# Performance work log

Measured on AMD Instinct MI355X. Metric: run time of the kernel, lower is better.

The kernel has to match this reference:

```python
import jax, jax.numpy as jnp
import numpy as np

MOE_TOPK = 2


def setup_inputs() -> dict:
    key = jax.random.key(0)
    k1, k2 = jax.random.split(key, 2)
    hidden_states = jax.random.normal(k1, (4, 4096, 2048), dtype=jnp.float32)
    gate_w = jax.random.normal(k2, (2048, 64), dtype=jnp.float32) * 0.02
    gate_b = jnp.zeros((64,), dtype=jnp.float32)
    return {"hidden_states": hidden_states, "gate_w": gate_w, "gate_b": gate_b}


def reference(hidden_states, gate_w, gate_b):
    # flatten [B, S, D] -> [N, D]
    x = hidden_states.reshape(-1, hidden_states.shape[-1])
    # gate linear: [N, E]
    logits = jnp.einsum("nd,de->ne", x, gate_w) + gate_b
    # stable softmax; torch detaches the max (no grad through max path)
    logits_max = jax.lax.stop_gradient(jnp.max(logits, axis=-1, keepdims=True))
    probs = jax.nn.softmax(logits - logits_max, axis=-1)
    # top-k selection + renormalize
    topk_vals, topk_idx = jax.lax.top_k(probs, MOE_TOPK)
    if MOE_TOPK == 1:
        norm_vals = jnp.ones_like(topk_vals)
    else:
        sum_vals = jnp.clip(jnp.sum(topk_vals, axis=-1, keepdims=True), 1e-6, None)
        norm_vals = topk_vals / sum_vals
    return logits, norm_vals, topk_idx
```

## Files before the change

kernel.cpp:

```cpp
#include <hip/hip_runtime.h>
#include <hip/hip_bf16.h>

#define NTOK 16384
#define DIM  2048
#define NE   64
#define TPB  32
#define NTILE 2
#define KG   8
#define KPW  (DIM / KG)
#define KSTEPS (KPW / 32)
#define NKS_ALL (DIM / 32)
#define LP   65

typedef __attribute__((ext_vector_type(8))) short  short8;
typedef __attribute__((ext_vector_type(4))) float  f32x4;

static __device__ __forceinline__ unsigned short f2bf(float f) {
    unsigned u = __float_as_uint(f);
    unsigned r = (u + 0x7fffu + ((u >> 16) & 1u)) >> 16;
    return (unsigned short)r;
}
static __device__ __forceinline__ float bf2f(unsigned short h) {
    return __uint_as_float(((unsigned)h) << 16);
}

static __device__ __forceinline__ void cvt_pair(float x0, float x1,
                                                unsigned& hi, unsigned& lo) {
    union { __hip_bfloat162 b; unsigned u; } h, l;
    h.b = __float22bfloat162_rn(float2{x0, x1});
    float h0 = __uint_as_float(h.u << 16);
    float h1 = __uint_as_float(h.u & 0xffff0000u);
    l.b = __float22bfloat162_rn(float2{x0 - h0, x1 - h1});
    hi = h.u; lo = l.u;
}

__global__ void pack_w(const float* __restrict__ W,
                       unsigned short* __restrict__ WH,
                       unsigned short* __restrict__ WL) {
    int idx = blockIdx.x * 256 + threadIdx.x;
    if (idx >= DIM * NE) return;
    int k = idx / NE, e = idx % NE;
    float w = W[idx];
    unsigned short h = f2bf(w);
    unsigned short l = f2bf(w - bf2f(h));
    int etile = e >> 4, col = e & 15;
    int kstep = k >> 5, lsub = (k >> 3) & 3, j = k & 7;
    size_t off = (((size_t)etile * NKS_ALL + kstep) * 64 + (lsub * 16 + col)) * 8 + j;
    WH[off] = h;
    WL[off] = l;
}

__global__ __launch_bounds__(512, 4) void router_mfma(
    const float* __restrict__ X,
    const unsigned short* __restrict__ WH,
    const unsigned short* __restrict__ WL,
    const float* __restrict__ B, float* __restrict__ out)
{
    __shared__ float red[KG][TPB][LP];
    __shared__ float lg[TPB][LP];

    const int tid  = threadIdx.x;
    const int lane = tid & 63;
    const int kg   = __builtin_amdgcn_readfirstlane(tid >> 6);
    const int t0   = blockIdx.x * TPB;

    const int arow = lane & 15;
    const int koff = (lane >> 4) * 8;

    const float* xp0 = X + (size_t)(t0 + arow) * DIM + kg * KPW + koff;
    const float* xp1 = xp0 + (size_t)16 * DIM;

    f32x4 acc[NTILE][4];
#pragma unroll
    for (int t = 0; t < NTILE; ++t)
#pragma unroll
        for (int et = 0; et < 4; ++et) acc[t][et] = (f32x4){0.f, 0.f, 0.f, 0.f};

#pragma unroll 2
    for (int s = 0; s < KSTEPS; ++s) {
        float4 xa0 = *(const float4*)(xp0 + s * 32);
        float4 xb0 = *(const float4*)(xp0 + s * 32 + 4);
        float4 xa1 = *(const float4*)(xp1 + s * 32);
        float4 xb1 = *(const float4*)(xp1 + s * 32 + 4);

        const int ks = kg * KSTEPS + s;
        short8 bh[4], bl[4];
#pragma unroll
        for (int et = 0; et < 4; ++et) {
            size_t foff = (((size_t)et * NKS_ALL + ks) * 64 + lane) * 8;
            bh[et] = *(const short8*)(WH + foff);
            bl[et] = *(const short8*)(WL + foff);
        }

        union { unsigned u[4]; short8 s8; } ah[NTILE], al[NTILE];
        cvt_pair(xa0.x, xa0.y, ah[0].u[0], al[0].u[0]);
        cvt_pair(xa0.z, xa0.w, ah[0].u[1], al[0].u[1]);
        cvt_pair(xb0.x, xb0.y, ah[0].u[2], al[0].u[2]);
        cvt_pair(xb0.z, xb0.w, ah[0].u[3], al[0].u[3]);
        cvt_pair(xa1.x, xa1.y, ah[1].u[0], al[1].u[0]);
        cvt_pair(xa1.z, xa1.w, ah[1].u[1], al[1].u[1]);
        cvt_pair(xb1.x, xb1.y, ah[1].u[2], al[1].u[2]);
        cvt_pair(xb1.z, xb1.w, ah[1].u[3], al[1].u[3]);

#pragma unroll
        for (int et = 0; et < 4; ++et) {
#pragma unroll
            for (int t = 0; t < NTILE; ++t) {
                acc[t][et] = __builtin_amdgcn_mfma_f32_16x16x32_bf16(ah[t].s8, bh[et], acc[t][et], 0, 0, 0);
                acc[t][et] = __builtin_amdgcn_mfma_f32_16x16x32_bf16(ah[t].s8, bl[et], acc[t][et], 0, 0, 0);
                acc[t][et] = __builtin_amdgcn_mfma_f32_16x16x32_bf16(al[t].s8, bh[et], acc[t][et], 0, 0, 0);
            }
        }
    }

#pragma unroll
    for (int t = 0; t < NTILE; ++t)
#pragma unroll
        for (int et = 0; et < 4; ++et)
#pragma unroll
            for (int r = 0; r < 4; ++r)
                red[kg][t * 16 + (lane >> 4) * 4 + r][et * 16 + (lane & 15)] = acc[t][et][r];
    __syncthreads();

    float* out_nv  = out + (size_t)NTOK * NE;
    float* out_idx = out_nv + (size_t)NTOK * 2;

    {
        const int rt = tid >> 4;
        const int re = (tid & 15) * 4;
        float4 s = {0.f, 0.f, 0.f, 0.f};
#pragma unroll
        for (int g = 0; g < KG; ++g) {
            s.x += red[g][rt][re + 0];
            s.y += red[g][rt][re + 1];
            s.z += red[g][rt][re + 2];
            s.w += red[g][rt][re + 3];
        }
        float4 bb = *(const float4*)(B + re);
        s.x += bb.x; s.y += bb.y; s.z += bb.z; s.w += bb.w;
        *(float4*)&out[(size_t)(t0 + rt) * NE + re] = s;
        lg[rt][re + 0] = s.x;
        lg[rt][re + 1] = s.y;
        lg[rt][re + 2] = s.z;
        lg[rt][re + 3] = s.w;
    }
    __syncthreads();

    if (tid < TPB) {
        float m1 = -1e30f, m2 = -1e30f;
        int   i1 = 0, i2 = 0;
        for (int e = 0; e < NE; ++e) {
            float v = lg[tid][e];
            if (v > m1)      { m2 = m1; i2 = i1; m1 = v; i1 = e; }
            else if (v > m2) { m2 = v;  i2 = e; }
        }
        float e2  = expf(m2 - m1);
        float inv = 1.f / (1.f + e2);
        int t = t0 + tid;
        out_nv[t * 2 + 0]  = inv;
        out_nv[t * 2 + 1]  = e2 * inv;
        out_idx[t * 2 + 0] = (float)i1;
        out_idx[t * 2 + 1] = (float)i2;
    }
}

extern "C" void kernel_launch(void* const* d_in, const int* in_sizes, int n_in,
                              void* d_out, int out_size, void* d_ws, size_t ws_size,
                              hipStream_t stream) {
    const float* X = (const float*)d_in[0];
    const float* W = (const float*)d_in[1];
    const float* B = (const float*)d_in[2];
    float* out = (float*)d_out;

    unsigned short* WH = (unsigned short*)d_ws;
    unsigned short* WL = WH + (size_t)DIM * NE;

    hipLaunchKernelGGL(pack_w, dim3((DIM * NE + 255) / 256), dim3(256), 0, stream, W, WH, WL);
    hipLaunchKernelGGL(router_mfma, dim3(NTOK / TPB), dim3(512), 0, stream, X, WH, WL, B, out);
}
```

Before: 41.92 us.

## Double tokens per block and parallelize top-2 selection with lane shuffles

Each block now handles 64 tokens with 1024 threads: 16 waves split as 8 K-groups by 2 token halves, each computing its own 32-token slab. The final top-2 scan is split across 4 threads per token, each scanning 16 experts, then merged with xor shuffles including index tie-breaking. The aims are to cut block count and per-block overhead and to shorten the serial top-k tail. The cost is a much larger LDS footprint of about 150KB per block, which limits a CU to one block and may reduce the ability to overlap blocks.

```diff
diff --git a/kernel.cpp b/kernel.cpp
--- a/kernel.cpp
+++ b/kernel.cpp
@@ -4,7 +4,7 @@
 #define NTOK 16384
 #define DIM  2048
 #define NE   64
-#define TPB  32
+#define TPB  64
 #define NTILE 2
 #define KG   8
 #define KPW  (DIM / KG)
@@ -50,7 +50,7 @@
     WL[off] = l;
 }
 
-__global__ __launch_bounds__(512, 4) void router_mfma(
+__global__ __launch_bounds__(1024, 4) void router_mfma(
     const float* __restrict__ X,
     const unsigned short* __restrict__ WH,
     const unsigned short* __restrict__ WL,
@@ -61,13 +61,15 @@
 
     const int tid  = threadIdx.x;
     const int lane = tid & 63;
-    const int kg   = __builtin_amdgcn_readfirstlane(tid >> 6);
+    const int wv   = tid >> 6;
+    const int kg   = __builtin_amdgcn_readfirstlane(wv & 7);
+    const int th   = __builtin_amdgcn_readfirstlane(wv >> 3);
     const int t0   = blockIdx.x * TPB;
 
     const int arow = lane & 15;
     const int koff = (lane >> 4) * 8;
 
-    const float* xp0 = X + (size_t)(t0 + arow) * DIM + kg * KPW + koff;
+    const float* xp0 = X + (size_t)(t0 + th * 32 + arow) * DIM + kg * KPW + koff;
     const float* xp1 = xp0 + (size_t)16 * DIM;
 
     f32x4 acc[NTILE][4];
@@ -119,7 +121,7 @@
         for (int et = 0; et < 4; ++et)
 #pragma unroll
             for (int r = 0; r < 4; ++r)
-                red[kg][t * 16 + (lane >> 4) * 4 + r][et * 16 + (lane & 15)] = acc[t][et][r];
+                red[kg][th * 32 + t * 16 + (lane >> 4) * 4 + r][et * 16 + (lane & 15)] = acc[t][et][r];
     __syncthreads();
 
     float* out_nv  = out + (size_t)NTOK * NE;
@@ -146,21 +148,41 @@
     }
     __syncthreads();
 
-    if (tid < TPB) {
+    if (tid < 4 * TPB) {
+        const int tt = tid >> 2;
+        const int q  = tid & 3;
         float m1 = -1e30f, m2 = -1e30f;
         int   i1 = 0, i2 = 0;
-        for (int e = 0; e < NE; ++e) {
-            float v = lg[tid][e];
+#pragma unroll
+        for (int j = 0; j < 16; ++j) {
+            int   e = q * 16 + j;
+            float v = lg[tt][e];
             if (v > m1)      { m2 = m1; i2 = i1; m1 = v; i1 = e; }
             else if (v > m2) { m2 = v;  i2 = e; }
         }
-        float e2  = expf(m2 - m1);
-        float inv = 1.f / (1.f + e2);
-        int t = t0 + tid;
-        out_nv[t * 2 + 0]  = inv;
-        out_nv[t * 2 + 1]  = e2 * inv;
-        out_idx[t * 2 + 0] = (float)i1;
-        out_idx[t * 2 + 1] = (float)i2;
+#pragma unroll
+        for (int d = 1; d <= 2; d <<= 1) {
+            float om1 = __shfl_xor(m1, d);
+            int   oi1 = __shfl_xor(i1, d);
+            float om2 = __shfl_xor(m2, d);
+            int   oi2 = __shfl_xor(i2, d);
+            bool agt = (m1 > om1) || (m1 == om1 && i1 < oi1);
+            float a1 = agt ? m1 : om1;  int ai1 = agt ? i1 : oi1;
+            float c2 = agt ? m2 : om2;  int ci2 = agt ? i2 : oi2;
+            float c1 = agt ? om1 : m1;  int ci1 = agt ? oi1 : i1;
+            bool sgt = (c2 > c1) || (c2 == c1 && ci2 < ci1);
+            m1 = a1; i1 = ai1;
+            m2 = sgt ? c2 : c1; i2 = sgt ? ci2 : ci1;
+        }
+        if (q == 0) {
+            float e2  = expf(m2 - m1);
+            float inv = 1.f / (1.f + e2);
+            int t = t0 + tt;
+            out_nv[t * 2 + 0]  = inv;
+            out_nv[t * 2 + 1]  = e2 * inv;
+            out_idx[t * 2 + 0] = (float)i1;
+            out_idx[t * 2 + 1] = (float)i2;
+        }
     }
 }
 
@@ -176,5 +198,5 @@
     unsigned short* WL = WH + (size_t)DIM * NE;
 
     hipLaunchKernelGGL(pack_w, dim3((DIM * NE + 255) / 256), dim3(256), 0, stream, W, WH, WL);
-    hipLaunchKernelGGL(router_mfma, dim3(NTOK / TPB), dim3(512), 0, stream, X, WH, WL, B, out);
-}
+    hipLaunchKernelGGL(router_mfma, dim3(NTOK / TPB), dim3(1024), 0, stream, X, WH, WL, B, out);
+}
```

After: 38.79 us. 1.08x faster.
